# Kernel tuning notes

Measured on AMD Instinct MI355X. Metric: run time of the kernel, lower is better.

The kernel has to match this reference:

```python
import jax, jax.numpy as jnp
import numpy as np

D = 256; NH = 8; NL = 4; NP = 4; DH = D // NH; DFFN = 1024; EPS = 1e-5
SHAPES = [(100, 100), (50, 50), (25, 25), (13, 13)]  # (H, W) per level
STARTS = np.cumsum([0] + [h * w for h, w in SHAPES]).tolist()
TOT = STARTS[-1]  # 13294


def layernorm(x, g, b):
    m = x.mean(-1, keepdims=True)
    v = ((x - m) ** 2).mean(-1, keepdims=True)
    return (x - m) / jnp.sqrt(v + EPS) * g + b


def mha(q, k, v, in_w, in_b, out_w, out_b):
    # q,k,v: (nq, bs, D); torch nn.MultiheadAttention semantics
    nq, bs, _ = q.shape
    wq, wk, wv = in_w[:D], in_w[D:2 * D], in_w[2 * D:]
    bq, bk, bv = in_b[:D], in_b[D:2 * D], in_b[2 * D:]
    qp = (q @ wq.T + bq).reshape(nq, bs, NH, DH)
    kp = (k @ wk.T + bk).reshape(k.shape[0], bs, NH, DH)
    vp = (v @ wv.T + bv).reshape(v.shape[0], bs, NH, DH)
    scores = jnp.einsum('qbhd,kbhd->bhqk', qp, kp) / jnp.sqrt(jnp.float32(DH))
    attn = jax.nn.softmax(scores, axis=-1)
    out = jnp.einsum('bhqk,kbhd->qbhd', attn, vp).reshape(nq, bs, D)
    return out @ out_w.T + out_b


def bilinear(img, x, y):
    # img: (B, H, W, C); x, y: (B, N) pixel coords; zero padding outside
    B, H, W, C = img.shape
    x0 = jnp.floor(x); y0 = jnp.floor(y)
    x0i = x0.astype(jnp.int32); y0i = y0.astype(jnp.int32)
    wx1 = x - x0; wx0 = 1.0 - wx1
    wy1 = y - y0; wy0 = 1.0 - wy1
    flat = img.reshape(B, H * W, C)

    def gather(xi, yi):
        valid = (xi >= 0) & (xi < W) & (yi >= 0) & (yi < H)
        idx = jnp.clip(yi, 0, H - 1) * W + jnp.clip(xi, 0, W - 1)
        v = jnp.take_along_axis(flat, idx[..., None], axis=1)
        return v * valid[..., None]

    return (gather(x0i, y0i) * (wx0 * wy0)[..., None]
            + gather(x0i + 1, y0i) * (wx1 * wy0)[..., None]
            + gather(x0i, y0i + 1) * (wx0 * wy1)[..., None]
            + gather(x0i + 1, y0i + 1) * (wx1 * wy1)[..., None])


def ms_deform(value, loc, attw):
    # value: (bs, len, NH, DH); loc: (bs, nq, NH, NL, NP, 2) normalized [0,1];
    # attw: (bs, nq, NH, NL, NP)
    bs, nq = loc.shape[0], loc.shape[1]
    out = jnp.zeros((bs, nq, NH, DH), value.dtype)
    for l, (Hl, Wl) in enumerate(SHAPES):
        vl = value[:, STARTS[l]:STARTS[l + 1]].reshape(bs, Hl, Wl, NH, DH)
        vl = vl.transpose(0, 3, 1, 2, 4).reshape(bs * NH, Hl, Wl, DH)
        ll = loc[:, :, :, l]  # (bs, nq, NH, NP, 2)
        # grid_sample align_corners=False: pixel = loc * size - 0.5
        x = (ll[..., 0] * Wl - 0.5).transpose(0, 2, 1, 3).reshape(bs * NH, nq * NP)
        y = (ll[..., 1] * Hl - 0.5).transpose(0, 2, 1, 3).reshape(bs * NH, nq * NP)
        samp = bilinear(vl, x, y).reshape(bs, NH, nq, NP, DH)
        out = out + jnp.einsum('bqhp,bhqpd->bqhd', attw[:, :, :, l], samp)
    return out.reshape(bs, nq, D)


def setup_inputs() -> dict:
    key = jax.random.key(0)
    ks = jax.random.split(key, 16)
    nq, bs = 900, 8
    s = 0.02
    W = lambda k, shape: jax.random.normal(k, shape, jnp.float32) * s
    return dict(
        tgt=jax.random.normal(ks[0], (nq, bs, D), jnp.float32),
        tgt_query_pos=jax.random.normal(ks[1], (nq, bs, D), jnp.float32),
        tgt_reference_points=jax.random.uniform(ks[2], (nq, bs, NL, 2), jnp.float32),
        memory=jax.random.normal(ks[3], (TOT, bs, D), jnp.float32),
        memory_spatial_shapes=jnp.array(SHAPES, jnp.int32),
        memory_level_start_index=jnp.array(STARTS[:-1], jnp.int32),
        sa_in_w=W(ks[4], (3 * D, D)), sa_in_b=jnp.zeros((3 * D,), jnp.float32),
        sa_out_w=W(ks[5], (D, D)), sa_out_b=jnp.zeros((D,), jnp.float32),
        norm1_g=jnp.ones((D,), jnp.float32), norm1_b=jnp.zeros((D,), jnp.float32),
        norm2_g=jnp.ones((D,), jnp.float32), norm2_b=jnp.zeros((D,), jnp.float32),
        norm3_g=jnp.ones((D,), jnp.float32), norm3_b=jnp.zeros((D,), jnp.float32),
        samp_w=W(ks[6], (NH * NL * NP * 2, D)),
        samp_b=jax.random.uniform(ks[7], (NH * NL * NP * 2,), jnp.float32, -0.5, 0.5),
        attw_w=W(ks[8], (NH * NL * NP, D)), attw_b=jnp.zeros((NH * NL * NP,), jnp.float32),
        val_w=W(ks[9], (D, D)), val_b=jnp.zeros((D,), jnp.float32),
        outp_w=W(ks[10], (D, D)), outp_b=jnp.zeros((D,), jnp.float32),
        lin1_w=W(ks[11], (DFFN, D)), lin1_b=jnp.zeros((DFFN,), jnp.float32),
        lin2_w=W(ks[12], (D, DFFN)), lin2_b=jnp.zeros((D,), jnp.float32),
    )


def reference(tgt, tgt_query_pos, tgt_reference_points, memory,
              memory_spatial_shapes, memory_level_start_index,
              sa_in_w, sa_in_b, sa_out_w, sa_out_b,
              norm1_g, norm1_b, norm2_g, norm2_b, norm3_g, norm3_b,
              samp_w, samp_b, attw_w, attw_b, val_w, val_b, outp_w, outp_b,
              lin1_w, lin1_b, lin2_w, lin2_b):
    nq, bs, _ = tgt.shape
    # --- self attention ---
    q = tgt + tgt_query_pos
    tgt = layernorm(tgt + mha(q, q, tgt, sa_in_w, sa_in_b, sa_out_w, sa_out_b),
                    norm2_g, norm2_b)
    # --- MS deformable cross attention ---
    q2 = (tgt + tgt_query_pos).transpose(1, 0, 2)          # (bs, nq, D)
    ref = tgt_reference_points.transpose(1, 0, 2, 3)       # (bs, nq, NL, 2)
    mem = memory.transpose(1, 0, 2)                        # (bs, len, D)
    value = (mem @ val_w.T + val_b).reshape(bs, TOT, NH, DH)
    off = (q2 @ samp_w.T + samp_b).reshape(bs, nq, NH, NL, NP, 2)
    aw = jax.nn.softmax((q2 @ attw_w.T + attw_b).reshape(bs, nq, NH, NL * NP), -1)
    aw = aw.reshape(bs, nq, NH, NL, NP)
    # offset normalizer = (W, H) per level
    normalizer = jnp.array([[w, h] for h, w in SHAPES], jnp.float32)
    loc = ref[:, :, None, :, None, :] + off / normalizer[None, None, None, :, None, :]
    ca = ms_deform(value, loc, aw) @ outp_w.T + outp_b      # (bs, nq, D)
    tgt = layernorm(tgt + ca.transpose(1, 0, 2), norm1_g, norm1_b)
    # --- FFN ---
    ffn = jax.nn.relu(tgt @ lin1_w.T + lin1_b) @ lin2_w.T + lin2_b
    return layernorm(tgt + ffn, norm3_g, norm3_b)
```

## Files before the change

### kernel.cpp

```cpp
#include <hip/hip_runtime.h>

#define NQ_   900
#define NT_   7200
#define TOT_  13294
#define MV_   106352

typedef __attribute__((ext_vector_type(8))) short short8;
typedef __attribute__((ext_vector_type(4))) float f32x4;

__device__ __forceinline__ ushort f2bf(float f) {
  union { float f; unsigned u; } v; v.f = f;
  unsigned r = (v.u + 0x7FFF + ((v.u >> 16) & 1)) >> 16;
  return (ushort)r;
}
__device__ __forceinline__ float bf2f(ushort u) {
  union { unsigned u; float f; } v; v.u = ((unsigned)u) << 16;
  return v.f;
}
__device__ __forceinline__ void stv(float* p, float v) { *p = v; }
__device__ __forceinline__ void stv(ushort* p, float v) { *p = f2bf(v); }

#define GLOAD_LDS16(g, l)                                            \
  __builtin_amdgcn_global_load_lds(                                  \
      (const __attribute__((address_space(1))) void*)(g),            \
      (__attribute__((address_space(3))) void*)(l), 16, 0, 0)

__global__ __launch_bounds__(256) void cvtw_k(ushort* __restrict__ dst,
    const float* s0, const float* s1, const float* s2, const float* s3,
    const float* s4, const float* s5, const float* s6, const float* s7) {
  for (int i = blockIdx.x * 256 + threadIdx.x; i < 237568; i += gridDim.x * 256) {
    const float* src; int base;
    if      (i < 32768)  { src = s0; base = 0; }
    else if (i < 49152)  { src = s1; base = 32768; }
    else if (i < 65536)  { src = s2; base = 49152; }
    else if (i < 73728)  { src = s3; base = 65536; }
    else if (i < 90112)  { src = s4; base = 73728; }
    else if (i < 106496) { src = s5; base = 90112; }
    else if (i < 172032) { src = s6; base = 106496; }
    else                 { src = s7; base = 172032; }
    float4 v = reinterpret_cast<const float4*>(src)[i - base];
    ushort4 r; r.x = f2bf(v.x); r.y = f2bf(v.y); r.z = f2bf(v.z); r.w = f2bf(v.w);
    reinterpret_cast<ushort4*>(dst)[i] = r;
  }
}

template <int BN, int AMODE, int OMODE, typename CT>
__global__ __launch_bounds__(BN * 2) void g2(
    const void* __restrict__ Av, const float* __restrict__ A2,
    const ushort* __restrict__ W, const float* __restrict__ bias,
    const float* __restrict__ bias2, const float* __restrict__ res,
    CT* __restrict__ C, void* __restrict__ C2v, int M, int N, int K) {
  constexpr int T = BN * 2;
  constexpr int WC = BN / 64;
  constexpr int NA = (128 * 32) / (T * 8);
  __shared__ ushort Alds[128 * 32];
  __shared__ ushort Blds[BN * 32];
  const int tid = threadIdx.x;
  const int w = tid >> 6, l = tid & 63;
  const int lr = l & 15, lg = l >> 4;
  const int m0 = blockIdx.y * 128, n0 = blockIdx.x * BN;
  const int wr = (w / WC) * 64, wc = (w % WC) * 64;
  f32x4 acc[4][4] = {};

  const int srow = tid >> 2;
  const int scol = (tid & 3) * 8;

  for (int k0 = 0; k0 < K; k0 += 32) {
    __syncthreads();
#pragma unroll
    for (int c = 0; c < 2; ++c) {
      int r = n0 + c * (T / 4) + srow;
      GLOAD_LDS16(W + (size_t)r * K + k0 + scol, &Blds[(c * (T / 4) + w * 16) * 32]);
    }
    if constexpr (AMODE == 0) {
#pragma unroll
      for (int c = 0; c < NA; ++c) {
        int r = m0 + c * (T / 4) + srow;
        if (r >= M) r = M - 1;
        GLOAD_LDS16((const ushort*)Av + (size_t)r * K + k0 + scol,
                    &Alds[(c * (T / 4) + w * 16) * 32]);
      }
    } else {
#pragma unroll
      for (int c = 0; c < NA; ++c) {
        int row = c * (T / 4) + srow;
        int gr = m0 + row; if (gr >= M) gr = M - 1;
        const float* ap = (const float*)Av + (size_t)gr * K + k0 + scol;
        float4 v0 = *reinterpret_cast<const float4*>(ap);
        float4 v1 = *reinterpret_cast<const float4*>(ap + 4);
        if constexpr (AMODE == 2) {
          const float* pp = A2 + (size_t)gr * K + k0 + scol;
          float4 p0 = *reinterpret_cast<const float4*>(pp);
          float4 p1 = *reinterpret_cast<const float4*>(pp + 4);
          v0.x += p0.x; v0.y += p0.y; v0.z += p0.z; v0.w += p0.w;
          v1.x += p1.x; v1.y += p1.y; v1.z += p1.z; v1.w += p1.w;
        }
        ushort tmp[8] = {f2bf(v0.x), f2bf(v0.y), f2bf(v0.z), f2bf(v0.w),
                         f2bf(v1.x), f2bf(v1.y), f2bf(v1.z), f2bf(v1.w)};
        *reinterpret_cast<short8*>(&Alds[row * 32 + scol]) =
            *reinterpret_cast<short8*>(tmp);
      }
    }
    __syncthreads();

    short8 af[4], bfr[4];
#pragma unroll
    for (int mi = 0; mi < 4; ++mi)
      af[mi] = *reinterpret_cast<const short8*>(&Alds[(wr + mi * 16 + lr) * 32 + lg * 8]);
#pragma unroll
    for (int ni = 0; ni < 4; ++ni)
      bfr[ni] = *reinterpret_cast<const short8*>(&Blds[(wc + ni * 16 + lr) * 32 + lg * 8]);
#pragma unroll
    for (int mi = 0; mi < 4; ++mi)
#pragma unroll
      for (int ni = 0; ni < 4; ++ni)
        acc[mi][ni] = __builtin_amdgcn_mfma_f32_16x16x32_bf16(af[mi], bfr[ni], acc[mi][ni], 0, 0, 0);
  }

#pragma unroll
  for (int mi = 0; mi < 4; ++mi)
#pragma unroll
    for (int ni = 0; ni < 4; ++ni) {
      int gn = n0 + wc + ni * 16 + lr;
      float bv = (OMODE == 7) ? (gn < 256 ? bias[gn] : bias2[gn - 256]) : bias[gn];
      f32x4 v = acc[mi][ni];
#pragma unroll
      for (int r = 0; r < 4; ++r) {
        int gm = m0 + wr + mi * 16 + lg * 4 + r;
        if (gm >= M) continue;
        float cv = v[r] + bv;
        if constexpr (OMODE == 0) {
          stv(&C[(size_t)gm * N + gn], cv);
        } else if constexpr (OMODE == 1) {
          cv += res[(size_t)gm * N + gn];
          stv(&C[(size_t)gm * N + gn], cv);
        } else if constexpr (OMODE == 2) {
          cv = fmaxf(cv, 0.f);
          stv(&C[(size_t)gm * N + gn], cv);
        } else if constexpr (OMODE == 4) {
          int q = gm >> 3, b = gm & 7;
          if (gn < 256) {
            int h = gn >> 5, d = gn & 31;
            ((ushort*)C)[(((size_t)b * 8 + h) * 1024 + q) * 32 + d] = f2bf(cv);
          } else {
            int gg = gn - 256, h = gg >> 5, d = gg & 31;
            ((ushort*)C2v)[(((size_t)b * 8 + h) * 960 + q) * 32 + d] = f2bf(cv);
          }
        } else if constexpr (OMODE == 5) {
          int q = gm >> 3, b = gm & 7, h = gn >> 5, d = gn & 31;
          ((ushort*)C)[(((size_t)b * 8 + h) * 960 + q) * 32 + d] = f2bf(cv);
        } else if constexpr (OMODE == 6) {
          int s = gm >> 3, b = gm & 7;
          ((ushort*)C)[((size_t)b * TOT_ + s) * 256 + gn] = f2bf(cv);
        } else if constexpr (OMODE == 7) {
          if (gn < 256) ((float*)C)[(size_t)gm * 256 + gn] = cv;
          else          ((float*)C2v)[(size_t)gm * 128 + gn - 256] = cv;
        }
      }
    }
}

__global__ __launch_bounds__(256) void attn_mfma(
    const ushort* __restrict__ Q, const ushort* __restrict__ Kt,
    const ushort* __restrict__ Vt, ushort* __restrict__ O) {
  const int qt = blockIdx.x, pr = blockIdx.y;
  const int b = pr >> 3, h = pr & 7;
  const int tid = threadIdx.x, w = tid >> 6, l = tid & 63;
  const int lr = l & 15, lg = l >> 4;
  const int qbase = qt * 128 + w * 32;
  const float SC = 0.17677669529663687f;

  __shared__ ushort Klds[64 * 32];
  __shared__ ushort Vlds[32 * 64];
  __shared__ ushort Plds[4 * 32 * 64];

  short8 qf[2];
#pragma unroll
  for (int nf = 0; nf < 2; ++nf) {
    int q = qbase + nf * 16 + lr;
    qf[nf] = *reinterpret_cast<const short8*>(&Q[((size_t)pr * 1024 + q) * 32 + lg * 8]);
  }
  f32x4 ot[2][2] = {};
  float mrow[2] = {-1e30f, -1e30f};
  float lsum[2] = {0.f, 0.f};

  for (int kt = 0; kt < 15; ++kt) {
    const int kv0 = kt * 64;
    __syncthreads();
    {
      int row = tid >> 2, s = tid & 3;
      short8 kv8 = *reinterpret_cast<const short8*>(
          &Kt[((size_t)pr * 960 + kv0 + row) * 32 + s * 8]);
      int s2 = s ^ ((row >> 1) & 3);
      *reinterpret_cast<short8*>(&Klds[row * 32 + s2 * 8]) = kv8;
      ushort tmp[8];
      *reinterpret_cast<short8*>(tmp) = *reinterpret_cast<const short8*>(
          &Vt[((size_t)pr * 960 + kv0 + row) * 32 + s * 8]);
      int slot = row >> 3;
#pragma unroll
      for (int j = 0; j < 8; ++j) {
        int d = s * 8 + j;
        Vlds[d * 64 + (slot ^ (d & 7)) * 8 + (row & 7)] = tmp[j];
      }
    }
    __syncthreads();

    short8 kf[4];
#pragma unroll
    for (int mf = 0; mf < 4; ++mf) {
      int row = mf * 16 + lr;
      int s2 = lg ^ ((row >> 1) & 3);
      kf[mf] = *reinterpret_cast<const short8*>(&Klds[row * 32 + s2 * 8]);
    }
    f32x4 sf[4][2];
    __builtin_amdgcn_s_setprio(1);
#pragma unroll
    for (int mf = 0; mf < 4; ++mf)
#pragma unroll
      for (int nf = 0; nf < 2; ++nf) {
        f32x4 z = {0.f, 0.f, 0.f, 0.f};
        sf[mf][nf] = __builtin_amdgcn_mfma_f32_16x16x32_bf16(kf[mf], qf[nf], z, 0, 0, 0);
      }
    __builtin_amdgcn_s_setprio(0);

#pragma unroll
    for (int nf = 0; nf < 2; ++nf) {
      float tm = -1e30f;
#pragma unroll
      for (int mf = 0; mf < 4; ++mf)
#pragma unroll
        for (int r = 0; r < 4; ++r) {
          float s = sf[mf][nf][r] * SC;
          int kv = kv0 + mf * 16 + lg * 4 + r;
          if (kv >= NQ_) s = -1e30f;
          sf[mf][nf][r] = s;
          tm = fmaxf(tm, s);
        }
      tm = fmaxf(tm, __shfl_xor(tm, 16));
      tm = fmaxf(tm, __shfl_xor(tm, 32));
      float mnew = fmaxf(mrow[nf], tm);
      float c = __expf(mrow[nf] - mnew);
      mrow[nf] = mnew;
      float ps = 0.f;
      int q_local = nf * 16 + lr;
#pragma unroll
      for (int mf = 0; mf < 4; ++mf) {
        ushort4 pk;
        float p0 = __expf(sf[mf][nf][0] - mnew);
        float p1 = __expf(sf[mf][nf][1] - mnew);
        float p2 = __expf(sf[mf][nf][2] - mnew);
        float p3 = __expf(sf[mf][nf][3] - mnew);
        ps += p0 + p1 + p2 + p3;
        pk.x = f2bf(p0); pk.y = f2bf(p1); pk.z = f2bf(p2); pk.w = f2bf(p3);
        int kvl = mf * 16 + lg * 4;
        int s3 = (kvl >> 3) ^ (q_local & 7);
        *reinterpret_cast<ushort4*>(
            &Plds[w * 2048 + q_local * 64 + s3 * 8 + (kvl & 7)]) = pk;
      }
      lsum[nf] = lsum[nf] * c + ps;
#pragma unroll
      for (int mf = 0; mf < 2; ++mf)
#pragma unroll
        for (int r = 0; r < 4; ++r) ot[mf][nf][r] *= c;
    }

#pragma unroll
    for (int ks = 0; ks < 2; ++ks) {
      short8 va[2], pb[2];
#pragma unroll
      for (int mf = 0; mf < 2; ++mf) {
        int d = mf * 16 + lr;
        int s3 = (ks * 4 + lg) ^ (d & 7);
        va[mf] = *reinterpret_cast<const short8*>(&Vlds[d * 64 + s3 * 8]);
      }
#pragma unroll
      for (int nf = 0; nf < 2; ++nf) {
        int q_local = nf * 16 + lr;
        int s3 = (ks * 4 + lg) ^ (q_local & 7);
        pb[nf] = *reinterpret_cast<const short8*>(&Plds[w * 2048 + q_local * 64 + s3 * 8]);
      }
      __builtin_amdgcn_s_setprio(1);
#pragma unroll
      for (int mf = 0; mf < 2; ++mf)
#pragma unroll
        for (int nf = 0; nf < 2; ++nf)
          ot[mf][nf] = __builtin_amdgcn_mfma_f32_16x16x32_bf16(va[mf], pb[nf], ot[mf][nf], 0, 0, 0);
      __builtin_amdgcn_s_setprio(0);
    }
  }

#pragma unroll
  for (int nf = 0; nf < 2; ++nf) {
    float ls = lsum[nf];
    ls += __shfl_xor(ls, 16);
    ls += __shfl_xor(ls, 32);
    float inv = 1.f / ls;
    int q = qbase + nf * 16 + lr;
    if (q < NQ_) {
#pragma unroll
      for (int mf = 0; mf < 2; ++mf) {
        ushort4 pk;
        pk.x = f2bf(ot[mf][nf][0] * inv); pk.y = f2bf(ot[mf][nf][1] * inv);
        pk.z = f2bf(ot[mf][nf][2] * inv); pk.w = f2bf(ot[mf][nf][3] * inv);
        int d0 = mf * 16 + lg * 4;
        *reinterpret_cast<ushort4*>(&O[((size_t)q * 8 + b) * 256 + h * 32 + d0]) = pk;
      }
    }
  }
}

__global__ __launch_bounds__(256) void deform_k(const ushort* __restrict__ val,
                                                const float* __restrict__ off,
                                                const float* __restrict__ awraw,
                                                const float* __restrict__ ref,
                                                ushort* __restrict__ out) {
  const int t0 = blockIdx.x * 4;
  const int tid = threadIdx.x;
  __shared__ float sx[4][128], sy[4][128], sw[4][128];
  const int LH[4] = {100, 50, 25, 13};
  const int LS[4] = {0, 10000, 12500, 13125};

  for (int e = tid; e < 512; e += 256) {
    int tt = e >> 7, lp = e & 127;
    int t = t0 + tt;
    int lvl = (lp >> 2) & 3;
    float ox = off[(size_t)t * 256 + lp * 2 + 0];
    float oy = off[(size_t)t * 256 + lp * 2 + 1];
    float rx = ref[((size_t)t * 4 + lvl) * 2 + 0];
    float ry = ref[((size_t)t * 4 + lvl) * 2 + 1];
    sx[tt][lp] = rx * (float)LH[lvl] + ox - 0.5f;
    sy[tt][lp] = ry * (float)LH[lvl] + oy - 0.5f;
    sw[tt][lp] = awraw[(size_t)t * 128 + lp];
  }
  __syncthreads();
  if (tid < 32) {
    int tt = tid >> 3, h = tid & 7;
    float* p = &sw[tt][h * 16];
    float mx = -1e30f;
#pragma unroll
    for (int k = 0; k < 16; ++k) mx = fmaxf(mx, p[k]);
    float v[16], s = 0.f;
#pragma unroll
    for (int k = 0; k < 16; ++k) { v[k] = __expf(p[k] - mx); s += v[k]; }
    float inv = 1.f / s;
#pragma unroll
    for (int k = 0; k < 16; ++k) p[k] = v[k] * inv;
  }
  __syncthreads();

  const int tt = tid >> 6, u = tid & 63;
  const int h = u >> 3, d0 = (u & 7) * 4;
  const int t = t0 + tt, b = t & 7;
  float a0 = 0.f, a1 = 0.f, a2 = 0.f, a3 = 0.f;

#pragma unroll
  for (int lvl = 0; lvl < 4; ++lvl) {
    const int Hl = LH[lvl], st = LS[lvl];
#pragma unroll
    for (int p = 0; p < 4; ++p) {
      int lp = (h * 4 + lvl) * 4 + p;
      float x = sx[tt][lp], y = sy[tt][lp], a = sw[tt][lp];
      float xf = floorf(x), yf = floorf(y);
      int x0 = (int)xf, y0 = (int)yf;
      float wx1 = x - xf, wx0 = 1.f - wx1;
      float wy1 = y - yf, wy0 = 1.f - wy1;
      float s0 = 0.f, s1 = 0.f, s2 = 0.f, s3 = 0.f;
#pragma unroll
      for (int cy = 0; cy < 2; ++cy)
#pragma unroll
        for (int cx = 0; cx < 2; ++cx) {
          int xi = x0 + cx, yi = y0 + cy;
          if (xi < 0 || xi >= Hl || yi < 0 || yi >= Hl) continue;
          ushort4 v4 = *reinterpret_cast<const ushort4*>(
              &val[((size_t)b * TOT_ + st + yi * Hl + xi) * 256 + h * 32 + d0]);
          float wgt = (cx ? wx1 : wx0) * (cy ? wy1 : wy0);
          s0 += wgt * bf2f(v4.x); s1 += wgt * bf2f(v4.y);
          s2 += wgt * bf2f(v4.z); s3 += wgt * bf2f(v4.w);
        }
      a0 += a * s0; a1 += a * s1; a2 += a * s2; a3 += a * s3;
    }
  }
  ushort4 o4; o4.x = f2bf(a0); o4.y = f2bf(a1); o4.z = f2bf(a2); o4.w = f2bf(a3);
  *reinterpret_cast<ushort4*>(&out[(size_t)t * 256 + h * 32 + d0]) = o4;
}

__global__ __launch_bounds__(256) void ln_k(const float* __restrict__ z,
                                            const float* __restrict__ g,
                                            const float* __restrict__ be,
                                            float* __restrict__ out, int rows) {
  const int wv = threadIdx.x >> 6, lane = threadIdx.x & 63;
  const int row = blockIdx.x * 4 + wv;
  if (row >= rows) return;
  float4 v = *reinterpret_cast<const float4*>(&z[(size_t)row * 256 + lane * 4]);
  float s = v.x + v.y + v.z + v.w;
#pragma unroll
  for (int o = 32; o; o >>= 1) s += __shfl_xor(s, o);
  float mean = s * (1.f / 256.f);
  float dx = v.x - mean, dy = v.y - mean, dz = v.z - mean, dw = v.w - mean;
  float vs = dx * dx + dy * dy + dz * dz + dw * dw;
#pragma unroll
  for (int o = 32; o; o >>= 1) vs += __shfl_xor(vs, o);
  float rstd = rsqrtf(vs * (1.f / 256.f) + 1e-5f);
  float4 gg = *reinterpret_cast<const float4*>(&g[lane * 4]);
  float4 bb = *reinterpret_cast<const float4*>(&be[lane * 4]);
  float4 r;
  r.x = dx * rstd * gg.x + bb.x;
  r.y = dy * rstd * gg.y + bb.y;
  r.z = dz * rstd * gg.z + bb.z;
  r.w = dw * rstd * gg.w + bb.w;
  *reinterpret_cast<float4*>(&out[(size_t)row * 256 + lane * 4]) = r;
}

extern "C" void kernel_launch(void* const* d_in, const int* in_sizes, int n_in,
                              void* d_out, int out_size, void* d_ws, size_t ws_size,
                              hipStream_t stream) {
  const float* tgt    = (const float*)d_in[0];
  const float* pos    = (const float*)d_in[1];
  const float* refpts = (const float*)d_in[2];
  const float* memory = (const float*)d_in[3];
  const float* sa_in_b  = (const float*)d_in[7];
  const float* sa_out_b = (const float*)d_in[9];
  const float* norm1_g = (const float*)d_in[10];
  const float* norm1_b = (const float*)d_in[11];
  const float* norm2_g = (const float*)d_in[12];
  const float* norm2_b = (const float*)d_in[13];
  const float* norm3_g = (const float*)d_in[14];
  const float* norm3_b = (const float*)d_in[15];
  const float* samp_b = (const float*)d_in[17];
  const float* attw_b = (const float*)d_in[19];
  const float* val_b  = (const float*)d_in[21];
  const float* outp_b = (const float*)d_in[23];
  const float* lin1_b = (const float*)d_in[25];
  const float* lin2_b = (const float*)d_in[27];
  float* out = (float*)d_out;

  char* ws = (char*)d_ws;
  ushort* wbf  = (ushort*)(ws + 0);
  ushort* valb = (ushort*)(ws + 2097152);
  char*   S    = ws + 56549376;
  float*  bufC = (float*)(ws + 83812352);
  float*  bufD = (float*)(ws + 91185152);

  ushort* sa_in_bf  = wbf + 0;
  ushort* sa_out_bf = wbf + 131072;
  ushort* sampw_bf  = wbf + 196608;
  ushort* val_bf    = wbf + 294912;
  ushort* outp_bf   = wbf + 360448;
  ushort* lin1_bf   = wbf + 425984;
  ushort* lin2_bf   = wbf + 688128;

  ushort* Qatt = (ushort*)(S + 0);
  ushort* Katt = (ushort*)(S + 4194304);
  ushort* Vatt = (ushort*)(S + 8126464);
  ushort* O_bf = (ushort*)(S + 12058624);
  float*  offs = (float*)(S + 0);
  float*  awb  = (float*)(S + 7372800);
  ushort* dbuf = (ushort*)(S + 11059200);
  ushort* hid  = (ushort*)(S + 0);

  cvtw_k<<<928, 256, 0, stream>>>(wbf, (const float*)d_in[6], (const float*)d_in[8],
      (const float*)d_in[16], (const float*)d_in[18], (const float*)d_in[20],
      (const float*)d_in[22], (const float*)d_in[24], (const float*)d_in[26]);

  g2<256, 1, 6, ushort><<<dim3(1, 831), 512, 0, stream>>>(
      memory, nullptr, val_bf, val_b, nullptr, nullptr, valb, nullptr, MV_, 256, 256);

  g2<256, 2, 4, ushort><<<dim3(2, 57), 512, 0, stream>>>(
      tgt, pos, sa_in_bf, sa_in_b, nullptr, nullptr, Qatt, Katt, NT_, 512, 256);
  g2<128, 1, 5, ushort><<<dim3(2, 57), 256, 0, stream>>>(
      tgt, nullptr, sa_in_bf + 512 * 256, sa_in_b + 512, nullptr, nullptr,
      Vatt, nullptr, NT_, 256, 256);

  attn_mfma<<<dim3(8, 64), 256, 0, stream>>>(Qatt, Katt, Vatt, O_bf);

  g2<128, 0, 1, float><<<dim3(2, 57), 256, 0, stream>>>(
      O_bf, nullptr, sa_out_bf, sa_out_b, nullptr, tgt, bufC, nullptr, NT_, 256, 256);
  ln_k<<<1800, 256, 0, stream>>>(bufC, norm2_g, norm2_b, bufD, NT_);

  g2<128, 2, 7, float><<<dim3(3, 57), 256, 0, stream>>>(
      bufD, pos, sampw_bf, samp_b, attw_b, nullptr, offs, awb, NT_, 384, 256);

  deform_k<<<1800, 256, 0, stream>>>(valb, offs, awb, refpts, dbuf);

  g2<128, 0, 1, float><<<dim3(2, 57), 256, 0, stream>>>(
      dbuf, nullptr, outp_bf, outp_b, nullptr, bufD, bufC, nullptr, NT_, 256, 256);
  ln_k<<<1800, 256, 0, stream>>>(bufC, norm1_g, norm1_b, bufD, NT_);

  g2<256, 1, 2, ushort><<<dim3(4, 57), 512, 0, stream>>>(
      bufD, nullptr, lin1_bf, lin1_b, nullptr, nullptr, hid, nullptr, NT_, 1024, 256);
  g2<128, 0, 1, float><<<dim3(2, 57), 256, 0, stream>>>(
      hid, nullptr, lin2_bf, lin2_b, nullptr, bufD, bufC, nullptr, NT_, 256, 1024);
  ln_k<<<1800, 256, 0, stream>>>(bufC, norm3_g, norm3_b, out, NT_);
}
```

Before: 505.0 us.

## Prefetch fp32 A tiles, emit bf16 activations from layernorm, restructure value GEMM

The GEMM kernel now issues the fp32 A-operand loads for the next k-step into registers right after the barrier, so global latency overlaps the MFMA work. The layernorm kernels also write bf16 copies of their outputs (with the query position added where needed), which lets the sampling-offset and FFN1 GEMMs read bf16 through the direct LDS path instead of converting fp32 on the fly. The value projection becomes a 3D grid over batch with a 128-wide tile, writing directly in (b, s, d) layout. The costs are extra register pressure from prefetch buffers, extra bf16 writes in layernorm, and a reshuffled scratch layout.

```diff
diff --git a/kernel.cpp b/kernel.cpp
--- a/kernel.cpp
+++ b/kernel.cpp
@@ -59,11 +59,33 @@
   const int w = tid >> 6, l = tid & 63;
   const int lr = l & 15, lg = l >> 4;
   const int m0 = blockIdx.y * 128, n0 = blockIdx.x * BN;
+  const int bz = blockIdx.z;
   const int wr = (w / WC) * 64, wc = (w % WC) * 64;
   f32x4 acc[4][4] = {};
 
   const int srow = tid >> 2;
   const int scol = (tid & 3) * 8;
+
+  float4 pa0[NA], pa1[NA], pb0[NA], pb1[NA];
+
+  auto loadA = [&](int k0) {
+#pragma unroll
+    for (int c = 0; c < NA; ++c) {
+      int gr = m0 + c * (T / 4) + srow;
+      if (gr >= M) gr = M - 1;
+      size_t arow = (AMODE == 3) ? ((size_t)gr * 8 + bz) : (size_t)gr;
+      const float* ap = (const float*)Av + arow * K + k0 + scol;
+      pa0[c] = *reinterpret_cast<const float4*>(ap);
+      pa1[c] = *reinterpret_cast<const float4*>(ap + 4);
+      if constexpr (AMODE == 2) {
+        const float* pp = A2 + (size_t)gr * K + k0 + scol;
+        pb0[c] = *reinterpret_cast<const float4*>(pp);
+        pb1[c] = *reinterpret_cast<const float4*>(pp + 4);
+      }
+    }
+  };
+
+  if constexpr (AMODE != 0) loadA(0);
 
   for (int k0 = 0; k0 < K; k0 += 32) {
     __syncthreads();
@@ -84,16 +106,10 @@
 #pragma unroll
       for (int c = 0; c < NA; ++c) {
         int row = c * (T / 4) + srow;
-        int gr = m0 + row; if (gr >= M) gr = M - 1;
-        const float* ap = (const float*)Av + (size_t)gr * K + k0 + scol;
-        float4 v0 = *reinterpret_cast<const float4*>(ap);
-        float4 v1 = *reinterpret_cast<const float4*>(ap + 4);
+        float4 v0 = pa0[c], v1 = pa1[c];
         if constexpr (AMODE == 2) {
-          const float* pp = A2 + (size_t)gr * K + k0 + scol;
-          float4 p0 = *reinterpret_cast<const float4*>(pp);
-          float4 p1 = *reinterpret_cast<const float4*>(pp + 4);
-          v0.x += p0.x; v0.y += p0.y; v0.z += p0.z; v0.w += p0.w;
-          v1.x += p1.x; v1.y += p1.y; v1.z += p1.z; v1.w += p1.w;
+          v0.x += pb0[c].x; v0.y += pb0[c].y; v0.z += pb0[c].z; v0.w += pb0[c].w;
+          v1.x += pb1[c].x; v1.y += pb1[c].y; v1.z += pb1[c].z; v1.w += pb1[c].w;
         }
         ushort tmp[8] = {f2bf(v0.x), f2bf(v0.y), f2bf(v0.z), f2bf(v0.w),
                          f2bf(v1.x), f2bf(v1.y), f2bf(v1.z), f2bf(v1.w)};
@@ -102,6 +118,9 @@
       }
     }
     __syncthreads();
+    if constexpr (AMODE != 0) {
+      if (k0 + 32 < K) loadA(k0 + 32);
+    }
 
     short8 af[4], bfr[4];
 #pragma unroll
@@ -149,12 +168,11 @@
         } else if constexpr (OMODE == 5) {
           int q = gm >> 3, b = gm & 7, h = gn >> 5, d = gn & 31;
           ((ushort*)C)[(((size_t)b * 8 + h) * 960 + q) * 32 + d] = f2bf(cv);
-        } else if constexpr (OMODE == 6) {
-          int s = gm >> 3, b = gm & 7;
-          ((ushort*)C)[((size_t)b * TOT_ + s) * 256 + gn] = f2bf(cv);
         } else if constexpr (OMODE == 7) {
           if (gn < 256) ((float*)C)[(size_t)gm * 256 + gn] = cv;
           else          ((float*)C2v)[(size_t)gm * 128 + gn - 256] = cv;
+        } else if constexpr (OMODE == 8) {
+          ((ushort*)C)[((size_t)bz * TOT_ + gm) * 256 + gn] = f2bf(cv);
         }
       }
     }
@@ -384,10 +402,13 @@
   *reinterpret_cast<ushort4*>(&out[(size_t)t * 256 + h * 32 + d0]) = o4;
 }
 
+template <int MODE>
 __global__ __launch_bounds__(256) void ln_k(const float* __restrict__ z,
                                             const float* __restrict__ g,
                                             const float* __restrict__ be,
-                                            float* __restrict__ out, int rows) {
+                                            float* __restrict__ out,
+                                            const float* __restrict__ pos,
+                                            ushort* __restrict__ aux, int rows) {
   const int wv = threadIdx.x >> 6, lane = threadIdx.x & 63;
   const int row = blockIdx.x * 4 + wv;
   if (row >= rows) return;
@@ -409,6 +430,17 @@
   r.z = dz * rstd * gg.z + bb.z;
   r.w = dw * rstd * gg.w + bb.w;
   *reinterpret_cast<float4*>(&out[(size_t)row * 256 + lane * 4]) = r;
+  if constexpr (MODE == 1) {
+    float4 pv = *reinterpret_cast<const float4*>(&pos[(size_t)row * 256 + lane * 4]);
+    ushort4 a;
+    a.x = f2bf(r.x + pv.x); a.y = f2bf(r.y + pv.y);
+    a.z = f2bf(r.z + pv.z); a.w = f2bf(r.w + pv.w);
+    *reinterpret_cast<ushort4*>(&aux[(size_t)row * 256 + lane * 4]) = a;
+  } else if constexpr (MODE == 2) {
+    ushort4 a;
+    a.x = f2bf(r.x); a.y = f2bf(r.y); a.z = f2bf(r.z); a.w = f2bf(r.w);
+    *reinterpret_cast<ushort4*>(&aux[(size_t)row * 256 + lane * 4]) = a;
+  }
 }
 
 extern "C" void kernel_launch(void* const* d_in, const int* in_sizes, int n_in,
@@ -453,17 +485,19 @@
   ushort* Katt = (ushort*)(S + 4194304);
   ushort* Vatt = (ushort*)(S + 8126464);
   ushort* O_bf = (ushort*)(S + 12058624);
-  float*  offs = (float*)(S + 0);
-  float*  awb  = (float*)(S + 7372800);
-  ushort* dbuf = (ushort*)(S + 11059200);
-  ushort* hid  = (ushort*)(S + 0);
+  ushort* q2bf = (ushort*)(S + 0);
+  float*  offs = (float*)(S + 3686400);
+  float*  awb  = (float*)(S + 11059200);
+  ushort* dbuf = (ushort*)(S + 15745024);
+  ushort* t2bf = (ushort*)(S + 0);
+  ushort* hid  = (ushort*)(S + 3686400);
 
   cvtw_k<<<928, 256, 0, stream>>>(wbf, (const float*)d_in[6], (const float*)d_in[8],
       (const float*)d_in[16], (const float*)d_in[18], (const float*)d_in[20],
       (const float*)d_in[22], (const float*)d_in[24], (const float*)d_in[26]);
 
-  g2<256, 1, 6, ushort><<<dim3(1, 831), 512, 0, stream>>>(
-      memory, nullptr, val_bf, val_b, nullptr, nullptr, valb, nullptr, MV_, 256, 256);
+  g2<128, 3, 8, ushort><<<dim3(2, 104, 8), 256, 0, stream>>>(
+      memory, nullptr, val_bf, val_b, nullptr, nullptr, valb, nullptr, TOT_, 256, 256);
 
   g2<256, 2, 4, ushort><<<dim3(2, 57), 512, 0, stream>>>(
       tgt, pos, sa_in_bf, sa_in_b, nullptr, nullptr, Qatt, Katt, NT_, 512, 256);
@@ -475,20 +509,20 @@
 
   g2<128, 0, 1, float><<<dim3(2, 57), 256, 0, stream>>>(
       O_bf, nullptr, sa_out_bf, sa_out_b, nullptr, tgt, bufC, nullptr, NT_, 256, 256);
-  ln_k<<<1800, 256, 0, stream>>>(bufC, norm2_g, norm2_b, bufD, NT_);
-
-  g2<128, 2, 7, float><<<dim3(3, 57), 256, 0, stream>>>(
-      bufD, pos, sampw_bf, samp_b, attw_b, nullptr, offs, awb, NT_, 384, 256);
+  ln_k<1><<<1800, 256, 0, stream>>>(bufC, norm2_g, norm2_b, bufD, pos, q2bf, NT_);
+
+  g2<128, 0, 7, float><<<dim3(3, 57), 256, 0, stream>>>(
+      q2bf, nullptr, sampw_bf, samp_b, attw_b, nullptr, offs, awb, NT_, 384, 256);
 
   deform_k<<<1800, 256, 0, stream>>>(valb, offs, awb, refpts, dbuf);
 
   g2<128, 0, 1, float><<<dim3(2, 57), 256, 0, stream>>>(
       dbuf, nullptr, outp_bf, outp_b, nullptr, bufD, bufC, nullptr, NT_, 256, 256);
-  ln_k<<<1800, 256, 0, stream>>>(bufC, norm1_g, norm1_b, bufD, NT_);
-
-  g2<256, 1, 2, ushort><<<dim3(4, 57), 512, 0, stream>>>(
-      bufD, nullptr, lin1_bf, lin1_b, nullptr, nullptr, hid, nullptr, NT_, 1024, 256);
+  ln_k<2><<<1800, 256, 0, stream>>>(bufC, norm1_g, norm1_b, bufD, nullptr, t2bf, NT_);
+
+  g2<256, 0, 2, ushort><<<dim3(4, 57), 512, 0, stream>>>(
+      t2bf, nullptr, lin1_bf, lin1_b, nullptr, nullptr, hid, nullptr, NT_, 1024, 256);
   g2<128, 0, 1, float><<<dim3(2, 57), 256, 0, stream>>>(
       hid, nullptr, lin2_bf, lin2_b, nullptr, bufD, bufC, nullptr, NT_, 256, 1024);
-  ln_k<<<1800, 256, 0, stream>>>(bufC, norm3_g, norm3_b, out, NT_);
-}
+  ln_k<0><<<1800, 256, 0, stream>>>(bufC, norm3_g, norm3_b, out, nullptr, nullptr, NT_);
+}
```

Result: no change. 504.2 us (-0.2%).
